# Kernel tuning notes

Measured on AMD Instinct MI355X. Metric: run time of the kernel, lower is better.

Reference implementation:

```python
import math
import jax, jax.numpy as jnp
import numpy as np

FACTOR = 2  # init kwarg of AutoCorrelation


def setup_inputs() -> dict:
    key0 = jax.random.key(0)
    kq, kk, kv = jax.random.split(key0, 3)
    B, H, L, D = 8, 8, 2048, 64
    return {
        "query": jax.random.normal(kq, (B, H, L, D), dtype=jnp.float32),
        "key": jax.random.normal(kk, (B, H, L, D), dtype=jnp.float32),
        "value": jax.random.normal(kv, (B, H, L, D), dtype=jnp.float32),
    }


def reference(query, key, value):
    # Inference (eval-mode) path of AutoCorrelation.forward.
    B, H, L, D = query.shape
    L_KV = key.shape[2]
    # _pad_or_truncate_key_value: match key/value length to query length
    if L > L_KV:
        pad = [(0, 0), (0, 0), (0, L - L_KV), (0, 0)]
        key = jnp.pad(key, pad)
        value = jnp.pad(value, pad)
    else:
        key = key[:, :, :L, :]
        value = value[:, :, :L, :]

    # _period_based_dependency: circular cross-correlation via FFT
    qf = jnp.fft.rfft(jnp.swapaxes(query, -2, -1), axis=-1)   # (B,H,D,L//2+1) complex
    kf = jnp.fft.rfft(jnp.swapaxes(key, -2, -1), axis=-1)
    corr = jnp.fft.irfft(qf * jnp.conj(kf), n=L, axis=-1)     # (B,H,D,L)

    # _time_delay_aggregation (eval branch: per-batch topk delays)
    mean_corr = corr.mean(axis=(1, 2))                         # (B,L)
    num_delays = min(FACTOR * math.ceil(math.log(L)), L)
    w, delay_idx = jax.lax.top_k(mean_corr, num_delays)       # (B,k)
    w = jax.nn.softmax(w, axis=-1)

    ar = jnp.arange(L)

    def body(ctx, inp):
        d, wk = inp  # (B,), (B,)
        idx = (ar[None, :] + d[:, None]) % L                   # (B,L) — circular shift == gather from doubled value
        gathered = jnp.take_along_axis(
            value, jnp.broadcast_to(idx[:, None, :, None], value.shape), axis=2
        )                                                      # (B,H,L,D)
        return ctx + wk[:, None, None, None] * gathered, None

    ctx0 = jnp.zeros_like(value)
    context, _ = jax.lax.scan(body, ctx0, (delay_idx.T, w.T))
    return context
```

## Files before the change

kernel.cpp:

```cpp
#include <hip/hip_runtime.h>

static constexpr int LSEQ = 2048;
static constexpr int NB   = 8;
static constexpr int NH   = 8;
static constexpr int ND   = 64;
static constexpr int NDEL = 16;

static constexpr size_t WS_S_OFF     = 0;
static constexpr size_t WS_W_OFF     = 131072;
static constexpr size_t WS_DELAY_OFF = 131584;

__device__ __forceinline__ int SW(int i) {
    return i ^ ((i >> 2) & 24) ^ ((i >> 6) & 6);
}

__global__ __launch_bounds__(256) void fft_corr(const float* __restrict__ q,
                                                const float* __restrict__ k,
                                                float2* __restrict__ S) {
    __shared__ float lds[8 * 2048];
    const int tid  = threadIdx.x;
    const int bi   = blockIdx.x;
    const int xcd  = bi & 7;
    const int slot = bi >> 3;
    const int bh   = xcd * 8 + (slot >> 4);
    const int dq   = slot & 15;
    const int b    = bh >> 3;
    const size_t base = (size_t)bh * LSEQ * ND + (size_t)(dq * 4);

    float4 qv[8], kv[8];
    #pragma unroll
    for (int u = 0; u < 8; ++u) {
        const int t = tid + 256 * u;
        qv[u] = *(const float4*)(q + base + (size_t)t * ND);
        kv[u] = *(const float4*)(k + base + (size_t)t * ND);
    }
    #pragma unroll
    for (int u = 0; u < 8; ++u) {
        const int s1 = SW(tid + 256 * u);
        #pragma unroll
        for (int c = 0; c < 4; ++c) {
            lds[(c << 11)       | (s1 ^ c)]       = (&qv[u].x)[c];
            lds[((c + 4) << 11) | (s1 ^ (c + 4))] = (&kv[u].x)[c];
        }
    }
    __syncthreads();

    const int ch   = tid >> 6;
    const int lane = tid & 63;
    const int reb  = ch << 11;
    const int imb  = (ch + 4) << 11;
    const int rex  = ch;
    const int imx  = ch + 4;

    #pragma unroll
    for (int s = 0; s < 4; ++s) {
        const int   lq = 9 - 2 * s;
        const int   qq = 1 << lq;
        const float w0 = -6.28318530717958647692f / (float)(qq << 2);
        #pragma unroll
        for (int u = 0; u < 8; ++u) {
            const int j  = lane + 64 * u;
            const int kk = j & (qq - 1);
            const int i0 = ((j >> lq) << (lq + 2)) | kk;
            const int s0 = SW(i0), sA = SW(i0 + qq), sB = SW(i0 + 2 * qq), sC = SW(i0 + 3 * qq);
            const int r0 = reb | (s0 ^ rex), r1 = reb | (sA ^ rex),
                      r2 = reb | (sB ^ rex), r3 = reb | (sC ^ rex);
            const int m0 = imb | (s0 ^ imx), m1 = imb | (sA ^ imx),
                      m2 = imb | (sB ^ imx), m3 = imb | (sC ^ imx);
            const float x0r = lds[r0], x0i = lds[m0], x1r = lds[r1], x1i = lds[m1];
            const float x2r = lds[r2], x2i = lds[m2], x3r = lds[r3], x3i = lds[m3];
            float sn, cs;
            __sincosf(w0 * (float)kk, &sn, &cs);
            const float c2 = cs * cs - sn * sn, s2 = 2.f * cs * sn;
            const float Ar = x0r + x2r, Ai = x0i + x2i;
            const float B0r = x0r - x2r, B0i = x0i - x2i;
            const float Cr = x1r + x3r, Ci = x1i + x3i;
            const float D0r = x1r - x3r, D0i = x1i - x3i;
            lds[r0] = Ar + Cr; lds[m0] = Ai + Ci;
            const float T1r = Ar - Cr, T1i = Ai - Ci;
            lds[r1] = T1r * c2 - T1i * s2; lds[m1] = T1r * s2 + T1i * c2;
            const float Br = B0r * cs - B0i * sn, Bi = B0r * sn + B0i * cs;
            const float Dr = D0r * sn + D0i * cs, Di = D0i * sn - D0r * cs;
            lds[r2] = Br + Dr; lds[m2] = Bi + Di;
            const float T3r = Br - Dr, T3i = Bi - Di;
            lds[r3] = T3r * c2 - T3i * s2; lds[m3] = T3r * s2 + T3i * c2;
        }
        __syncthreads();
    }

    const float RH = 0.70710678118654752440f;
    #pragma unroll
    for (int u = 0; u < 4; ++u) {
        const int pb = tid << 3;
        int rp[8], ip[8];
        #pragma unroll
        for (int c = 0; c < 8; ++c) {
            const int s1 = SW(pb + c);
            rp[c] = (u << 11) | (s1 ^ u);
            ip[c] = ((u + 4) << 11) | (s1 ^ (u + 4));
        }
        float er[8], ei[8];
        #pragma unroll
        for (int c = 0; c < 8; ++c) { er[c] = lds[rp[c]]; ei[c] = lds[ip[c]]; }
        float ur[4], ui[4], vr[4], vi[4];
        ur[0] = er[0] + er[4]; ui[0] = ei[0] + ei[4];
        vr[0] = er[0] - er[4]; vi[0] = ei[0] - ei[4];
        { const float a = er[1] - er[5], bq = ei[1] - ei[5];
          ur[1] = er[1] + er[5]; ui[1] = ei[1] + ei[5];
          vr[1] = RH * (a + bq); vi[1] = RH * (bq - a); }
        { const float a = er[2] - er[6], bq = ei[2] - ei[6];
          ur[2] = er[2] + er[6]; ui[2] = ei[2] + ei[6];
          vr[2] = bq; vi[2] = -a; }
        { const float a = er[3] - er[7], bq = ei[3] - ei[7];
          ur[3] = er[3] + er[7]; ui[3] = ei[3] + ei[7];
          vr[3] = RH * (bq - a); vi[3] = -RH * (a + bq); }
        {
            const float a0r = ur[0] + ur[2], a0i = ui[0] + ui[2];
            const float a2r = ur[0] - ur[2], a2i = ui[0] - ui[2];
            const float a1r = ur[1] + ur[3], a1i = ui[1] + ui[3];
            const float a3r = ui[1] - ui[3], a3i = -(ur[1] - ur[3]);
            lds[rp[0]] = a0r + a1r; lds[ip[0]] = a0i + a1i;
            lds[rp[1]] = a0r - a1r; lds[ip[1]] = a0i - a1i;
            lds[rp[2]] = a2r + a3r; lds[ip[2]] = a2i + a3i;
            lds[rp[3]] = a2r - a3r; lds[ip[3]] = a2i - a3i;
        }
        {
            const float a0r = vr[0] + vr[2], a0i = vi[0] + vi[2];
            const float a2r = vr[0] - vr[2], a2i = vi[0] - vi[2];
            const float a1r = vr[1] + vr[3], a1i = vi[1] + vi[3];
            const float a3r = vi[1] - vi[3], a3i = -(vr[1] - vr[3]);
            lds[rp[4]] = a0r + a1r; lds[ip[4]] = a0i + a1i;
            lds[rp[5]] = a0r - a1r; lds[ip[5]] = a0i - a1i;
            lds[rp[6]] = a2r + a3r; lds[ip[6]] = a2i + a3i;
            lds[rp[7]] = a2r - a3r; lds[ip[7]] = a2i - a3i;
        }
    }
    __syncthreads();

    #pragma unroll
    for (int u = 0; u < 8; ++u) {
        const int fb = (tid >> 6) * 8 + u;
        const int f  = fb + (lane << 5);
        const int m  = (2048 - f) & 2047;
        const int p  = (int)(__brev((unsigned)f) >> 21);
        const int pm = (int)(__brev((unsigned)m) >> 21);
        const int sf = SW(p), sm = SW(pm);
        float sr = 0.f, si = 0.f;
        #pragma unroll
        for (int c = 0; c < 4; ++c) {
            const float Zfx = lds[(c << 11) | (sf ^ c)];
            const float Zfy = lds[((c + 4) << 11) | (sf ^ (c + 4))];
            const float Zmx = lds[(c << 11) | (sm ^ c)];
            const float Zmy = lds[((c + 4) << 11) | (sm ^ (c + 4))];
            const float qr = 0.5f * (Zfx + Zmx), qi = 0.5f * (Zfy - Zmy);
            const float kr = 0.5f * (Zfy + Zmy), ki = 0.5f * (Zmx - Zfx);
            sr += qr * kr + qi * ki;
            si += qi * kr - qr * ki;
        }
        atomicAdd(&S[b * 2048 + p].x, sr);
        atomicAdd(&S[b * 2048 + p].y, si);
    }
}

__global__ __launch_bounds__(1024) void ifft_topk(const float2* __restrict__ S,
                                                  float* __restrict__ wout,
                                                  int* __restrict__ dout) {
    const int b = blockIdx.x, tid = threadIdx.x;
    __shared__ float2 y[LSEQ];
    __shared__ float  mc[LSEQ];
    __shared__ float  pv[16];
    __shared__ int    pi[16];
    __shared__ float  topv[NDEL];
    __shared__ int    topi[NDEL];

    y[tid]        = S[b * 2048 + tid];
    y[tid + 1024] = S[b * 2048 + tid + 1024];
    __syncthreads();

    for (int M = 2; M <= LSEQ; M <<= 1) {
        const int   half = M >> 1;
        const float w0   = 6.28318530717958647692f / (float)M;
        const int   kk = tid & (half - 1), i0 = 2 * tid - kk, i1 = i0 + half;
        const float2 a = y[i0], bb = y[i1];
        float sn, cs;
        __sincosf(w0 * (float)kk, &sn, &cs);
        const float tx = bb.x * cs - bb.y * sn, ty = bb.x * sn + bb.y * cs;
        y[i0] = make_float2(a.x + tx, a.y + ty);
        y[i1] = make_float2(a.x - tx, a.y - ty);
        __syncthreads();
    }

    const float scale = 1.0f / ((float)LSEQ * (float)(NH * ND));
    mc[tid]        = y[tid].x * scale;
    mc[tid + 1024] = y[tid + 1024].x * scale;
    __syncthreads();

    const int lane = tid & 63, wv = tid >> 6;
    for (int it = 0; it < NDEL; ++it) {
        const float v0 = mc[tid], v1 = mc[tid + 1024];
        float bv; int bix;
        if (v1 > v0) { bv = v1; bix = tid + 1024; } else { bv = v0; bix = tid; }
        #pragma unroll
        for (int off = 32; off; off >>= 1) {
            const float ov = __shfl_xor(bv, off);
            const int   oi = __shfl_xor(bix, off);
            if (ov > bv || (ov == bv && oi < bix)) { bv = ov; bix = oi; }
        }
        if (lane == 0) { pv[wv] = bv; pi[wv] = bix; }
        __syncthreads();
        if (tid < 64) {
            float v = (tid < 16) ? pv[tid] : -3e38f;
            int  ii = (tid < 16) ? pi[tid] : 0;
            #pragma unroll
            for (int off = 8; off; off >>= 1) {
                const float ov = __shfl_xor(v, off);
                const int   oi = __shfl_xor(ii, off);
                if (ov > v || (ov == v && oi < ii)) { v = ov; ii = oi; }
            }
            if (tid == 0) { topv[it] = v; topi[it] = ii; mc[ii] = -3e38f; }
        }
        __syncthreads();
    }

    if (tid == 0) {
        const float m = topv[0];
        float e[NDEL], sum = 0.f;
        for (int t2 = 0; t2 < NDEL; ++t2) { e[t2] = __expf(topv[t2] - m); sum += e[t2]; }
        const float inv = 1.0f / sum;
        for (int t2 = 0; t2 < NDEL; ++t2) {
            wout[b * NDEL + t2] = e[t2] * inv;
            dout[b * NDEL + t2] = topi[t2];
        }
    }
}

__global__ __launch_bounds__(256) void gather_out(const float* __restrict__ v,
                                                  const float* __restrict__ w,
                                                  const int* __restrict__ delay,
                                                  float* __restrict__ out) {
    const int bi  = blockIdx.x;
    const int xcd = bi & 7;
    const int s   = bi >> 3;
    const int bh  = xcd * 8 + (s >> 7);
    const int bt  = s & 127;
    const int b   = bh >> 3;
    const int tid = threadIdx.x;

    __shared__ float sw_[NDEL];
    __shared__ int   sd_[NDEL];
    if (tid < NDEL) {
        sw_[tid] = w[b * NDEL + tid];
        sd_[tid] = delay[b * NDEL + tid];
    }
    __syncthreads();

    const float* vb = v + (size_t)bh * LSEQ * ND;
    float*       ob = out + (size_t)bh * LSEQ * ND;

    const int row = tid >> 4;
    const int col = (tid & 15) * 4;
    const int t   = bt * 16 + row;

    float4 acc = make_float4(0.f, 0.f, 0.f, 0.f);
    #pragma unroll
    for (int kk = 0; kk < NDEL; ++kk) {
        const int r = (t + sd_[kk]) & (LSEQ - 1);
        const float4 vv = *(const float4*)(vb + (size_t)r * ND + col);
        const float wv = sw_[kk];
        acc.x += wv * vv.x; acc.y += wv * vv.y;
        acc.z += wv * vv.z; acc.w += wv * vv.w;
    }
    *(float4*)(ob + (size_t)t * ND + col) = acc;
}

extern "C" void kernel_launch(void* const* d_in, const int* in_sizes, int n_in,
                              void* d_out, int out_size, void* d_ws, size_t ws_size,
                              hipStream_t stream) {
    const float* q = (const float*)d_in[0];
    const float* k = (const float*)d_in[1];
    const float* v = (const float*)d_in[2];
    float* out = (float*)d_out;

    float2* S     = (float2*)((char*)d_ws + WS_S_OFF);
    float*  w     = (float*)((char*)d_ws + WS_W_OFF);
    int*    delay = (int*)((char*)d_ws + WS_DELAY_OFF);

    hipMemsetAsync(d_ws, 0, (size_t)NB * 2048 * sizeof(float2), stream);

    fft_corr<<<dim3(NB * NH * 16), dim3(256), 0, stream>>>(q, k, S);
    ifft_topk<<<dim3(NB), dim3(1024), 0, stream>>>(S, w, delay);
    gather_out<<<dim3(NB * NH * 128), dim3(256), 0, stream>>>(v, w, delay, out);
}
```

Measured before the change: 221.8 us.

## Process two column groups per FFT block and replace atomics with partial-sum reduction

Each fft_corr block now handles 8 columns in two rounds, prefetching the second half into registers while the first round runs, and accumulates the per-frequency correlation in registers. Block count drops from 1024 to 512. Twiddles are precomputed once into an LDS table instead of calling sincos per butterfly, and LDS data is stored as packed float2 with a new swizzle. The global atomicAdd accumulation and memset are replaced by writing 64 partial spectra to workspace plus a separate reduce_S kernel, which adds an extra launch and about 8 MB of traffic.

```diff
diff --git a/kernel.cpp b/kernel.cpp
--- a/kernel.cpp
+++ b/kernel.cpp
@@ -6,160 +6,202 @@
 static constexpr int ND   = 64;
 static constexpr int NDEL = 16;
 
-static constexpr size_t WS_S_OFF     = 0;
-static constexpr size_t WS_W_OFF     = 131072;
-static constexpr size_t WS_DELAY_OFF = 131584;
-
-__device__ __forceinline__ int SW(int i) {
-    return i ^ ((i >> 2) & 24) ^ ((i >> 6) & 6);
-}
+static constexpr size_t WS_P_OFF     = 0;
+static constexpr size_t WS_S_OFF     = 8388608;
+static constexpr size_t WS_W_OFF     = 8519680;
+static constexpr size_t WS_DELAY_OFF = 8520192;
+
+__device__ __forceinline__ int SW2(int j) { return j ^ ((j >> 4) & 15); }
 
 __global__ __launch_bounds__(256) void fft_corr(const float* __restrict__ q,
                                                 const float* __restrict__ k,
-                                                float2* __restrict__ S) {
-    __shared__ float lds[8 * 2048];
-    const int tid  = threadIdx.x;
-    const int bi   = blockIdx.x;
-    const int xcd  = bi & 7;
-    const int slot = bi >> 3;
-    const int bh   = xcd * 8 + (slot >> 4);
-    const int dq   = slot & 15;
-    const int b    = bh >> 3;
-    const size_t base = (size_t)bh * LSEQ * ND + (size_t)(dq * 4);
-
-    float4 qv[8], kv[8];
+                                                float2* __restrict__ P) {
+    __shared__ float2 z[4][LSEQ];
+    __shared__ float2 tw[680];
+
+    const int tid = threadIdx.x;
+    const int bi  = blockIdx.x;
+    const int xcd = bi & 7;
+    const int sl  = bi >> 3;
+    const int bh  = xcd * 8 + (sl >> 3);
+    const int grp = sl & 7;
+    const int b   = bh >> 3;
+    const int h   = bh & 7;
+    const size_t base = (size_t)bh * LSEQ * ND + (size_t)(grp * 8);
+
+    for (int i = tid; i < 680; i += 256) {
+        int idx, M;
+        if (i < 512)      { idx = i;       M = 2048; }
+        else if (i < 640) { idx = i - 512; M = 512; }
+        else if (i < 672) { idx = i - 640; M = 128; }
+        else              { idx = i - 672; M = 32; }
+        float sn, cs;
+        __sincosf(-6.28318530717958647692f * (float)idx / (float)M, &sn, &cs);
+        tw[i] = make_float2(cs, sn);
+    }
+
+    float4 qa[8], ka[8];
+    #pragma unroll
+    for (int u = 0; u < 8; ++u) {
+        const size_t r = base + (size_t)(tid + 256 * u) * ND;
+        qa[u] = *(const float4*)(q + r);
+        ka[u] = *(const float4*)(k + r);
+    }
     #pragma unroll
     for (int u = 0; u < 8; ++u) {
         const int t = tid + 256 * u;
-        qv[u] = *(const float4*)(q + base + (size_t)t * ND);
-        kv[u] = *(const float4*)(k + base + (size_t)t * ND);
-    }
+        #pragma unroll
+        for (int c = 0; c < 4; ++c)
+            z[c][SW2(t)] = make_float2((&qa[u].x)[c], (&ka[u].x)[c]);
+    }
+    float4 qb[8], kb[8];
     #pragma unroll
     for (int u = 0; u < 8; ++u) {
-        const int s1 = SW(tid + 256 * u);
-        #pragma unroll
-        for (int c = 0; c < 4; ++c) {
-            lds[(c << 11)       | (s1 ^ c)]       = (&qv[u].x)[c];
-            lds[((c + 4) << 11) | (s1 ^ (c + 4))] = (&kv[u].x)[c];
-        }
-    }
-    __syncthreads();
-
-    const int ch   = tid >> 6;
+        const size_t r = base + (size_t)(tid + 256 * u) * ND + 4;
+        qb[u] = *(const float4*)(q + r);
+        kb[u] = *(const float4*)(k + r);
+    }
+
+    float accR[8], accI[8];
+    #pragma unroll
+    for (int u = 0; u < 8; ++u) { accR[u] = 0.f; accI[u] = 0.f; }
+
     const int lane = tid & 63;
-    const int reb  = ch << 11;
-    const int imb  = (ch + 4) << 11;
-    const int rex  = ch;
-    const int imx  = ch + 4;
-
-    #pragma unroll
-    for (int s = 0; s < 4; ++s) {
-        const int   lq = 9 - 2 * s;
-        const int   qq = 1 << lq;
-        const float w0 = -6.28318530717958647692f / (float)(qq << 2);
+    const int wch  = tid >> 6;
+    const float RH = 0.70710678118654752440f;
+
+    for (int round = 0; round < 2; ++round) {
+        __syncthreads();
+
+        const int tb[4] = {0, 512, 640, 672};
+        #pragma unroll
+        for (int st = 0; st < 4; ++st) {
+            const int lq = 9 - 2 * st;
+            const int qq = 1 << lq;
+            const float2* twb = &tw[tb[st]];
+            #pragma unroll
+            for (int u = 0; u < 8; ++u) {
+                const int j  = lane + (u << 6);
+                const int kk = j & (qq - 1);
+                const int i0 = ((j >> lq) << (lq + 2)) | kk;
+                const float2 x0 = z[wch][SW2(i0)];
+                const float2 x1 = z[wch][SW2(i0 + qq)];
+                const float2 x2 = z[wch][SW2(i0 + 2 * qq)];
+                const float2 x3 = z[wch][SW2(i0 + 3 * qq)];
+                const float2 w1 = twb[kk];
+                const float cs = w1.x, sn = w1.y;
+                const float c2 = cs * cs - sn * sn, s2 = 2.f * cs * sn;
+                const float Ar = x0.x + x2.x, Ai = x0.y + x2.y;
+                const float B0r = x0.x - x2.x, B0i = x0.y - x2.y;
+                const float Cr = x1.x + x3.x, Ci = x1.y + x3.y;
+                const float D0r = x1.x - x3.x, D0i = x1.y - x3.y;
+                z[wch][SW2(i0)] = make_float2(Ar + Cr, Ai + Ci);
+                const float T1r = Ar - Cr, T1i = Ai - Ci;
+                z[wch][SW2(i0 + qq)] =
+                    make_float2(T1r * c2 - T1i * s2, T1r * s2 + T1i * c2);
+                const float Br = B0r * cs - B0i * sn, Bi = B0r * sn + B0i * cs;
+                const float Dr = D0r * sn + D0i * cs, Di = D0i * sn - D0r * cs;
+                z[wch][SW2(i0 + 2 * qq)] = make_float2(Br + Dr, Bi + Di);
+                const float T3r = Br - Dr, T3i = Bi - Di;
+                z[wch][SW2(i0 + 3 * qq)] =
+                    make_float2(T3r * c2 - T3i * s2, T3r * s2 + T3i * c2);
+            }
+            __syncthreads();
+        }
+
+        #pragma unroll
+        for (int c4 = 0; c4 < 4; ++c4) {
+            const int pb = tid << 3;
+            float2 e[8];
+            #pragma unroll
+            for (int c = 0; c < 8; ++c) e[c] = z[c4][SW2(pb | c)];
+            float ur[4], ui[4], vr[4], vi[4];
+            ur[0] = e[0].x + e[4].x; ui[0] = e[0].y + e[4].y;
+            vr[0] = e[0].x - e[4].x; vi[0] = e[0].y - e[4].y;
+            { const float a = e[1].x - e[5].x, bq = e[1].y - e[5].y;
+              ur[1] = e[1].x + e[5].x; ui[1] = e[1].y + e[5].y;
+              vr[1] = RH * (a + bq); vi[1] = RH * (bq - a); }
+            { const float a = e[2].x - e[6].x, bq = e[2].y - e[6].y;
+              ur[2] = e[2].x + e[6].x; ui[2] = e[2].y + e[6].y;
+              vr[2] = bq; vi[2] = -a; }
+            { const float a = e[3].x - e[7].x, bq = e[3].y - e[7].y;
+              ur[3] = e[3].x + e[7].x; ui[3] = e[3].y + e[7].y;
+              vr[3] = RH * (bq - a); vi[3] = -RH * (a + bq); }
+            {
+                const float a0r = ur[0] + ur[2], a0i = ui[0] + ui[2];
+                const float a2r = ur[0] - ur[2], a2i = ui[0] - ui[2];
+                const float a1r = ur[1] + ur[3], a1i = ui[1] + ui[3];
+                const float a3r = ui[1] - ui[3], a3i = -(ur[1] - ur[3]);
+                z[c4][SW2(pb | 0)] = make_float2(a0r + a1r, a0i + a1i);
+                z[c4][SW2(pb | 1)] = make_float2(a0r - a1r, a0i - a1i);
+                z[c4][SW2(pb | 2)] = make_float2(a2r + a3r, a2i + a3i);
+                z[c4][SW2(pb | 3)] = make_float2(a2r - a3r, a2i - a3i);
+            }
+            {
+                const float a0r = vr[0] + vr[2], a0i = vi[0] + vi[2];
+                const float a2r = vr[0] - vr[2], a2i = vi[0] - vi[2];
+                const float a1r = vr[1] + vr[3], a1i = vi[1] + vi[3];
+                const float a3r = vi[1] - vi[3], a3i = -(vr[1] - vr[3]);
+                z[c4][SW2(pb | 4)] = make_float2(a0r + a1r, a0i + a1i);
+                z[c4][SW2(pb | 5)] = make_float2(a0r - a1r, a0i - a1i);
+                z[c4][SW2(pb | 6)] = make_float2(a2r + a3r, a2i + a3i);
+                z[c4][SW2(pb | 7)] = make_float2(a2r - a3r, a2i - a3i);
+            }
+        }
+        __syncthreads();
+
         #pragma unroll
         for (int u = 0; u < 8; ++u) {
-            const int j  = lane + 64 * u;
-            const int kk = j & (qq - 1);
-            const int i0 = ((j >> lq) << (lq + 2)) | kk;
-            const int s0 = SW(i0), sA = SW(i0 + qq), sB = SW(i0 + 2 * qq), sC = SW(i0 + 3 * qq);
-            const int r0 = reb | (s0 ^ rex), r1 = reb | (sA ^ rex),
-                      r2 = reb | (sB ^ rex), r3 = reb | (sC ^ rex);
-            const int m0 = imb | (s0 ^ imx), m1 = imb | (sA ^ imx),
-                      m2 = imb | (sB ^ imx), m3 = imb | (sC ^ imx);
-            const float x0r = lds[r0], x0i = lds[m0], x1r = lds[r1], x1i = lds[m1];
-            const float x2r = lds[r2], x2i = lds[m2], x3r = lds[r3], x3i = lds[m3];
-            float sn, cs;
-            __sincosf(w0 * (float)kk, &sn, &cs);
-            const float c2 = cs * cs - sn * sn, s2 = 2.f * cs * sn;
-            const float Ar = x0r + x2r, Ai = x0i + x2i;
-            const float B0r = x0r - x2r, B0i = x0i - x2i;
-            const float Cr = x1r + x3r, Ci = x1i + x3i;
-            const float D0r = x1r - x3r, D0i = x1i - x3i;
-            lds[r0] = Ar + Cr; lds[m0] = Ai + Ci;
-            const float T1r = Ar - Cr, T1i = Ai - Ci;
-            lds[r1] = T1r * c2 - T1i * s2; lds[m1] = T1r * s2 + T1i * c2;
-            const float Br = B0r * cs - B0i * sn, Bi = B0r * sn + B0i * cs;
-            const float Dr = D0r * sn + D0i * cs, Di = D0i * sn - D0r * cs;
-            lds[r2] = Br + Dr; lds[m2] = Bi + Di;
-            const float T3r = Br - Dr, T3i = Bi - Di;
-            lds[r3] = T3r * c2 - T3i * s2; lds[m3] = T3r * s2 + T3i * c2;
-        }
-        __syncthreads();
-    }
-
-    const float RH = 0.70710678118654752440f;
-    #pragma unroll
-    for (int u = 0; u < 4; ++u) {
-        const int pb = tid << 3;
-        int rp[8], ip[8];
-        #pragma unroll
-        for (int c = 0; c < 8; ++c) {
-            const int s1 = SW(pb + c);
-            rp[c] = (u << 11) | (s1 ^ u);
-            ip[c] = ((u + 4) << 11) | (s1 ^ (u + 4));
-        }
-        float er[8], ei[8];
-        #pragma unroll
-        for (int c = 0; c < 8; ++c) { er[c] = lds[rp[c]]; ei[c] = lds[ip[c]]; }
-        float ur[4], ui[4], vr[4], vi[4];
-        ur[0] = er[0] + er[4]; ui[0] = ei[0] + ei[4];
-        vr[0] = er[0] - er[4]; vi[0] = ei[0] - ei[4];
-        { const float a = er[1] - er[5], bq = ei[1] - ei[5];
-          ur[1] = er[1] + er[5]; ui[1] = ei[1] + ei[5];
-          vr[1] = RH * (a + bq); vi[1] = RH * (bq - a); }
-        { const float a = er[2] - er[6], bq = ei[2] - ei[6];
-          ur[2] = er[2] + er[6]; ui[2] = ei[2] + ei[6];
-          vr[2] = bq; vi[2] = -a; }
-        { const float a = er[3] - er[7], bq = ei[3] - ei[7];
-          ur[3] = er[3] + er[7]; ui[3] = ei[3] + ei[7];
-          vr[3] = RH * (bq - a); vi[3] = -RH * (a + bq); }
-        {
-            const float a0r = ur[0] + ur[2], a0i = ui[0] + ui[2];
-            const float a2r = ur[0] - ur[2], a2i = ui[0] - ui[2];
-            const float a1r = ur[1] + ur[3], a1i = ui[1] + ui[3];
-            const float a3r = ui[1] - ui[3], a3i = -(ur[1] - ur[3]);
-            lds[rp[0]] = a0r + a1r; lds[ip[0]] = a0i + a1i;
-            lds[rp[1]] = a0r - a1r; lds[ip[1]] = a0i - a1i;
-            lds[rp[2]] = a2r + a3r; lds[ip[2]] = a2i + a3i;
-            lds[rp[3]] = a2r - a3r; lds[ip[3]] = a2i - a3i;
-        }
-        {
-            const float a0r = vr[0] + vr[2], a0i = vi[0] + vi[2];
-            const float a2r = vr[0] - vr[2], a2i = vi[0] - vi[2];
-            const float a1r = vr[1] + vr[3], a1i = vi[1] + vi[3];
-            const float a3r = vi[1] - vi[3], a3i = -(vr[1] - vr[3]);
-            lds[rp[4]] = a0r + a1r; lds[ip[4]] = a0i + a1i;
-            lds[rp[5]] = a0r - a1r; lds[ip[5]] = a0i - a1i;
-            lds[rp[6]] = a2r + a3r; lds[ip[6]] = a2i + a3i;
-            lds[rp[7]] = a2r - a3r; lds[ip[7]] = a2i - a3i;
-        }
-    }
-    __syncthreads();
-
+            const int fb = wch * 8 + u;
+            const int f  = fb | (lane << 5);
+            const int m  = (2048 - f) & 2047;
+            const int p  = (int)(__brev((unsigned)f) >> 21);
+            const int pm = (int)(__brev((unsigned)m) >> 21);
+            float sr = 0.f, si = 0.f;
+            #pragma unroll
+            for (int c = 0; c < 4; ++c) {
+                const float2 Zf = z[c][SW2(p)];
+                const float2 Zm = z[c][SW2(pm)];
+                const float qr = 0.5f * (Zf.x + Zm.x), qi = 0.5f * (Zf.y - Zm.y);
+                const float kr = 0.5f * (Zf.y + Zm.y), ki = 0.5f * (Zm.x - Zf.x);
+                sr += qr * kr + qi * ki;
+                si += qi * kr - qr * ki;
+            }
+            accR[u] += sr; accI[u] += si;
+        }
+
+        if (round == 0) {
+            __syncthreads();
+            #pragma unroll
+            for (int u = 0; u < 8; ++u) {
+                const int t = tid + 256 * u;
+                #pragma unroll
+                for (int c = 0; c < 4; ++c)
+                    z[c][SW2(t)] = make_float2((&qb[u].x)[c], (&kb[u].x)[c]);
+            }
+        }
+    }
+
+    const int part = h * 8 + grp;
+    float2* Pp = P + (size_t)part * (NB * 2048) + (size_t)b * 2048;
     #pragma unroll
     for (int u = 0; u < 8; ++u) {
-        const int fb = (tid >> 6) * 8 + u;
-        const int f  = fb + (lane << 5);
-        const int m  = (2048 - f) & 2047;
-        const int p  = (int)(__brev((unsigned)f) >> 21);
-        const int pm = (int)(__brev((unsigned)m) >> 21);
-        const int sf = SW(p), sm = SW(pm);
-        float sr = 0.f, si = 0.f;
-        #pragma unroll
-        for (int c = 0; c < 4; ++c) {
-            const float Zfx = lds[(c << 11) | (sf ^ c)];
-            const float Zfy = lds[((c + 4) << 11) | (sf ^ (c + 4))];
-            const float Zmx = lds[(c << 11) | (sm ^ c)];
-            const float Zmy = lds[((c + 4) << 11) | (sm ^ (c + 4))];
-            const float qr = 0.5f * (Zfx + Zmx), qi = 0.5f * (Zfy - Zmy);
-            const float kr = 0.5f * (Zfy + Zmy), ki = 0.5f * (Zmx - Zfx);
-            sr += qr * kr + qi * ki;
-            si += qi * kr - qr * ki;
-        }
-        atomicAdd(&S[b * 2048 + p].x, sr);
-        atomicAdd(&S[b * 2048 + p].y, si);
-    }
+        const int f = (wch * 8 + u) | (lane << 5);
+        const int p = (int)(__brev((unsigned)f) >> 21);
+        Pp[p] = make_float2(accR[u], accI[u]);
+    }
+}
+
+__global__ __launch_bounds__(256) void reduce_S(const float2* __restrict__ P,
+                                                float2* __restrict__ S) {
+    const int g = blockIdx.x * 256 + threadIdx.x;
+    float accx = 0.f, accy = 0.f;
+    #pragma unroll 8
+    for (int part = 0; part < 64; ++part) {
+        const float2 v = P[(size_t)part * (NB * 2048) + g];
+        accx += v.x; accy += v.y;
+    }
+    S[g] = make_float2(accx, accy);
 }
 
 __global__ __launch_bounds__(1024) void ifft_topk(const float2* __restrict__ S,
@@ -281,13 +323,13 @@
     const float* v = (const float*)d_in[2];
     float* out = (float*)d_out;
 
+    float2* P     = (float2*)((char*)d_ws + WS_P_OFF);
     float2* S     = (float2*)((char*)d_ws + WS_S_OFF);
     float*  w     = (float*)((char*)d_ws + WS_W_OFF);
     int*    delay = (int*)((char*)d_ws + WS_DELAY_OFF);
 
-    hipMemsetAsync(d_ws, 0, (size_t)NB * 2048 * sizeof(float2), stream);
-
-    fft_corr<<<dim3(NB * NH * 16), dim3(256), 0, stream>>>(q, k, S);
+    fft_corr<<<dim3(512), dim3(256), 0, stream>>>(q, k, P);
+    reduce_S<<<dim3(64), dim3(256), 0, stream>>>(P, S);
     ifft_topk<<<dim3(NB), dim3(1024), 0, stream>>>(S, w, delay);
     gather_out<<<dim3(NB * NH * 128), dim3(256), 0, stream>>>(v, w, delay, out);
 }
```

Result: slower. 226.9 us (+2.3%).
